# Kernel tuning notes

Hardware: AMD Instinct MI355X
Metric: run time of the kernel (lower is better)

The kernel has to match this reference:

```python
import jax, jax.numpy as jnp
import numpy as np

N = 100000   # nodes
E = 1000000  # edges
F = 64       # in_features == out_features
ALPHA = 0.2  # leaky-relu negative slope


def setup_inputs() -> dict:
    key = jax.random.key(0)
    k = jax.random.split(key, 6)
    h = jax.random.normal(k[0], (N, F), jnp.float32)
    W = jax.random.normal(k[1], (F, F), jnp.float32) * 0.1   # Linear weight [out,in]
    Wb = jnp.zeros((F,), jnp.float32)
    a = jax.random.normal(k[2], (2 * F,), jnp.float32) * 0.1  # attn vector (Linear(2F,1))
    ab = jnp.zeros((), jnp.float32)
    src = jax.random.randint(k[3], (E,), 0, N, dtype=jnp.int32)
    dst = jax.random.randint(k[4], (E,), 0, N, dtype=jnp.int32)
    return {"h": h, "W": W, "Wb": Wb, "a": a, "ab": ab, "src": src, "dst": dst}


def reference(h, W, Wb, a, ab, src, dst):
    # Wh = W(h)  (dropout is identity in eval mode / dropout=0)
    Wh = h @ W.T + Wb                                   # [N, F]
    # e = leakyrelu(a([Wh_src || Wh_dst])) ; split a to avoid concat
    a_src, a_dst = a[:F], a[F:]
    e = jax.nn.leaky_relu(Wh[src] @ a_src + Wh[dst] @ a_dst + ab, ALPHA)  # [E]
    # segment softmax over destination nodes (DGL mailbox softmax)
    m = jax.ops.segment_max(e, dst, num_segments=N)     # [N], -inf for empty
    m = jnp.where(jnp.isfinite(m), m, 0.0)
    ex = jnp.exp(e - m[dst])                            # [E]
    denom = jax.ops.segment_sum(ex, dst, num_segments=N)
    attn = ex / jnp.where(denom[dst] > 0, denom[dst], 1.0)
    # weighted scatter-sum of source features to destinations
    h_prime = jax.ops.segment_sum(attn[:, None] * Wh[src], dst, num_segments=N)  # [N, F]
    return h_prime
```

## Files before the change

kernel.cpp:

```cpp
#include <hip/hip_runtime.h>

#define NF 64
#define ALPHA 0.2f
#define BSH 7
#define BNODES 128
#define CAPG 2048
#define PB 4096
#define HB 800
#define NBIN 1024

typedef unsigned int  uint;
typedef unsigned short ushort;

typedef __attribute__((ext_vector_type(8))) short  short8;
typedef __attribute__((ext_vector_type(4))) float  floatx4;

__device__ __forceinline__ ushort f2bf(float x) {
    uint u = __float_as_uint(x);
    u += 0x7fffu + ((u >> 16) & 1u);
    return (ushort)(u >> 16);
}

__device__ __forceinline__ short8 pack8(float4 lo, float4 hi) {
    short8 r;
    r[0] = (short)f2bf(lo.x); r[1] = (short)f2bf(lo.y);
    r[2] = (short)f2bf(lo.z); r[3] = (short)f2bf(lo.w);
    r[4] = (short)f2bf(hi.x); r[5] = (short)f2bf(hi.y);
    r[6] = (short)f2bf(hi.z); r[7] = (short)f2bf(hi.w);
    return r;
}

__global__ __launch_bounds__(256) void wh_part_kernel(
    const float* __restrict__ h, const float* __restrict__ W,
    const float* __restrict__ Wb, const float* __restrict__ a,
    ushort* __restrict__ whbf, float* __restrict__ s_src, float* __restrict__ s_dst,
    const int* __restrict__ src, const int* __restrict__ dst,
    int* __restrict__ bctr, uint* __restrict__ tmp,
    int N, int E, int edgeB, int NB)
{
    __shared__ uint   stage[PB];
    __shared__ ushort bid[PB];
    __shared__ int    hist[HB];
    __shared__ int    lbase[HB];
    __shared__ int    ctr[HB];
    __shared__ int    gbase[HB];
    __shared__ int    sw[256];

    int t = threadIdx.x;

    if ((int)blockIdx.x < edgeB) {
        int base = (int)blockIdx.x * PB;
        int total = E - base; if (total > PB) total = PB; if (total < 0) total = 0;

        for (int i = t; i < HB; i += 256) hist[i] = 0;
        __syncthreads();

        uint pk[16]; int bb[16];
        #pragma unroll
        for (int g = 0; g < 4; ++g) {
            int ei = base + g * 1024 + t * 4;
            int s4[4], d4[4];
            if (ei + 3 < E) {
                int4 sv = *(const int4*)&src[ei];
                int4 dv = *(const int4*)&dst[ei];
                s4[0]=sv.x; s4[1]=sv.y; s4[2]=sv.z; s4[3]=sv.w;
                d4[0]=dv.x; d4[1]=dv.y; d4[2]=dv.z; d4[3]=dv.w;
            } else {
                #pragma unroll
                for (int j = 0; j < 4; ++j) {
                    int e = ei + j;
                    s4[j] = (e < E) ? src[e] : -1;
                    d4[j] = (e < E) ? dst[e] : -1;
                }
            }
            #pragma unroll
            for (int j = 0; j < 4; ++j) {
                int i16 = g * 4 + j;
                if (d4[j] >= 0) {
                    pk[i16] = ((uint)s4[j] << BSH) | (uint)(d4[j] & (BNODES - 1));
                    bb[i16] = d4[j] >> BSH;
                    atomicAdd(&hist[bb[i16]], 1);
                } else bb[i16] = -1;
            }
        }
        __syncthreads();

        int b0 = t * 4;
        int c0 = 0, c1 = 0, c2 = 0, c3 = 0;
        if (b0 < HB)     c0 = hist[b0];
        if (b0 + 1 < HB) c1 = hist[b0+1];
        if (b0 + 2 < HB) c2 = hist[b0+2];
        if (b0 + 3 < HB) c3 = hist[b0+3];
        int tsum = c0 + c1 + c2 + c3;
        sw[t] = tsum; __syncthreads();
        for (int off = 1; off < 256; off <<= 1) {
            int x = (t >= off) ? sw[t - off] : 0;
            __syncthreads();
            sw[t] += x;
            __syncthreads();
        }
        int ex = sw[t] - tsum;
        if (b0 < HB)     { lbase[b0]   = ex; ex += c0; }
        if (b0 + 1 < HB) { lbase[b0+1] = ex; ex += c1; }
        if (b0 + 2 < HB) { lbase[b0+2] = ex; ex += c2; }
        if (b0 + 3 < HB) { lbase[b0+3] = ex; }
        __syncthreads();

        for (int q = t; q < NB; q += 256) {
            int c = hist[q];
            gbase[q] = c ? atomicAdd(&bctr[q], c) : 0;
            ctr[q] = lbase[q];
        }
        __syncthreads();

        #pragma unroll
        for (int i = 0; i < 16; ++i) {
            if (bb[i] >= 0) {
                int pos = atomicAdd(&ctr[bb[i]], 1);
                stage[pos] = pk[i];
                bid[pos] = (ushort)bb[i];
            }
        }
        __syncthreads();

        for (int i = t; i < total; i += 256) {
            int q = bid[i];
            int off = gbase[q] + (i - lbase[q]);
            if (off < CAPG) tmp[(size_t)q * CAPG + off] = stage[i];
        }
        return;
    }

    int lane = t & 63;
    int wave = t >> 6;
    int r0   = ((int)blockIdx.x - edgeB) * 64 + wave * 16;
    if (r0 >= N) return;
    int m    = lane & 15;
    int quad = lane >> 4;

    short8 bfrag[4][2];
    #pragma unroll
    for (int ct = 0; ct < 4; ++ct) {
        const float* wrow = W + (size_t)(ct * 16 + m) * 64 + quad * 8;
        #pragma unroll
        for (int kh = 0; kh < 2; ++kh) {
            float4 lo = *(const float4*)(wrow + kh * 32);
            float4 hi = *(const float4*)(wrow + kh * 32 + 4);
            bfrag[ct][kh] = pack8(lo, hi);
        }
    }

    int row_a = r0 + m; if (row_a >= N) row_a = N - 1;
    const float* hrow = h + (size_t)row_a * 64 + quad * 8;
    floatx4 zero = {0.f, 0.f, 0.f, 0.f};
    floatx4 acc[4] = {zero, zero, zero, zero};
    #pragma unroll
    for (int kh = 0; kh < 2; ++kh) {
        float4 lo = *(const float4*)(hrow + kh * 32);
        float4 hi = *(const float4*)(hrow + kh * 32 + 4);
        short8 af = pack8(lo, hi);
        #pragma unroll
        for (int ct = 0; ct < 4; ++ct)
            acc[ct] = __builtin_amdgcn_mfma_f32_16x16x32_bf16(af, bfrag[ct][kh], acc[ct], 0, 0, 0);
    }

    float p1[4] = {0.f, 0.f, 0.f, 0.f}, p2[4] = {0.f, 0.f, 0.f, 0.f};
    #pragma unroll
    for (int ct = 0; ct < 4; ++ct) {
        int col = ct * 16 + m;
        float wb  = Wb[col];
        float av1 = a[col];
        float av2 = a[64 + col];
        #pragma unroll
        for (int reg = 0; reg < 4; ++reg) {
            int row = r0 + quad * 4 + reg;
            float v = acc[ct][reg] + wb;
            if (row < N) whbf[(size_t)row * 64 + col] = f2bf(v);
            p1[reg] += v * av1;
            p2[reg] += v * av2;
        }
    }
    #pragma unroll
    for (int off = 8; off >= 1; off >>= 1) {
        #pragma unroll
        for (int reg = 0; reg < 4; ++reg) {
            p1[reg] += __shfl_down(p1[reg], off, 16);
            p2[reg] += __shfl_down(p2[reg], off, 16);
        }
    }
    if (m == 0) {
        #pragma unroll
        for (int reg = 0; reg < 4; ++reg) {
            int row = r0 + quad * 4 + reg;
            if (row < N) { s_src[row] = p1[reg]; s_dst[row] = p2[reg]; }
        }
    }
}

__global__ __launch_bounds__(512) void bucket_aggregate(
    const uint* __restrict__ tmp, const int* __restrict__ bctr,
    const float* __restrict__ s_src, const float* __restrict__ s_dst,
    const float* __restrict__ ab, const ushort* __restrict__ whbf,
    float* __restrict__ out, int N)
{
    __shared__ uint  ssrc[CAPG];
    __shared__ float sexv[CAPG];
    __shared__ int   cnts[NBIN];
    __shared__ int   excl[NBIN + 1];
    __shared__ int   ctr[NBIN];
    __shared__ float sdl[BNODES];

    int t = threadIdx.x;
    int b = blockIdx.x;
    int n0 = b << BSH;
    int cnt = bctr[b]; if (cnt > CAPG) cnt = CAPG;
    float ab0 = ab[0];

    for (int i = t; i < NBIN; i += 512) cnts[i] = 0;
    if (t < BNODES) {
        sdl[t] = (n0 + t < N) ? s_dst[n0 + t] + ab0 : 0.f;
    }
    __syncthreads();

    uint held[4]; int nh = 0;
    #pragma unroll
    for (int j = 0; j < 4; ++j) {
        int idx = t + j * 512;
        if (idx < cnt) {
            uint v = tmp[(size_t)b * CAPG + idx];
            held[nh++] = v;
            int bin = ((v & (BNODES - 1)) << 3) | ((v >> 21) & 7);
            atomicAdd(&cnts[bin], 1);
        }
    }
    __syncthreads();

    if (t < 64) {
        int base16 = t * 16;
        int c[16]; int s = 0;
        #pragma unroll
        for (int k = 0; k < 16; ++k) { c[k] = cnts[base16 + k]; s += c[k]; }
        int incl = s;
        #pragma unroll
        for (int off = 1; off < 64; off <<= 1) {
            int x = __shfl_up(incl, off, 64);
            if (t >= off) incl += x;
        }
        int e = incl - s;
        #pragma unroll
        for (int k = 0; k < 16; ++k) { excl[base16 + k] = e; ctr[base16 + k] = e; e += c[k]; }
        if (t == 63) excl[NBIN] = e;
    }
    __syncthreads();

    #pragma unroll
    for (int j = 0; j < 4; ++j) {
        if (j < nh) {
            uint v = held[j];
            uint s = v >> BSH;
            int node = v & (BNODES - 1);
            float e = s_src[s] + sdl[node];
            e = e > 0.f ? e : ALPHA * e;
            float ex = __expf(e);
            int bin = (node << 3) | ((v >> 21) & 7);
            int pos = atomicAdd(&ctr[bin], 1);
            ssrc[pos] = s; sexv[pos] = ex;
        }
    }
    __syncthreads();

    int g = t >> 3, l8 = t & 7;
    int nlim = N - n0; if (nlim > BNODES) nlim = BNODES;
    int nodeA = g, nodeB = g + 64;
    bool hasA = nodeA < nlim, hasB = nodeB < nlim;

    int a0 = hasA ? excl[nodeA << 3] : 0, a1 = hasA ? excl[(nodeA << 3) + 8] : 0;
    int b0 = hasB ? excl[nodeB << 3] : 0, b1 = hasB ? excl[(nodeB << 3) + 8] : 0;
    int na = a1 - a0, nb = b1 - b0;
    int iters = na > nb ? na : nb;

    float fA[8] = {0.f,0.f,0.f,0.f,0.f,0.f,0.f,0.f};
    float fB[8] = {0.f,0.f,0.f,0.f,0.f,0.f,0.f,0.f};
    float dnA = 0.f, dnB = 0.f;

    if (iters > 0) {
        uint  sA = (na > 0) ? ssrc[a0] : 0u;
        float eA = (na > 0) ? sexv[a0] : 0.f;
        uint4 pA = ((const uint4*)(whbf + (size_t)sA * 64))[l8];
        uint  sB = (nb > 0) ? ssrc[b0] : 0u;
        float eB = (nb > 0) ? sexv[b0] : 0.f;
        uint4 pB = ((const uint4*)(whbf + (size_t)sB * 64))[l8];

        for (int i = 0; i < iters; ++i) {
            int ia = (i + 1 < na) ? a0 + i + 1 : a0;
            int ib = (i + 1 < nb) ? b0 + i + 1 : b0;
            uint  sAn = (i + 1 < na) ? ssrc[ia] : 0u; float eAn = (i + 1 < na) ? sexv[ia] : 0.f;
            uint  sBn = (i + 1 < nb) ? ssrc[ib] : 0u; float eBn = (i + 1 < nb) ? sexv[ib] : 0.f;
            uint4 pAn = ((const uint4*)(whbf + (size_t)sAn * 64))[l8];
            uint4 pBn = ((const uint4*)(whbf + (size_t)sBn * 64))[l8];

            fA[0] += eA * __uint_as_float(pA.x << 16);
            fA[1] += eA * __uint_as_float(pA.x & 0xffff0000u);
            fA[2] += eA * __uint_as_float(pA.y << 16);
            fA[3] += eA * __uint_as_float(pA.y & 0xffff0000u);
            fA[4] += eA * __uint_as_float(pA.z << 16);
            fA[5] += eA * __uint_as_float(pA.z & 0xffff0000u);
            fA[6] += eA * __uint_as_float(pA.w << 16);
            fA[7] += eA * __uint_as_float(pA.w & 0xffff0000u);
            dnA += eA;
            fB[0] += eB * __uint_as_float(pB.x << 16);
            fB[1] += eB * __uint_as_float(pB.x & 0xffff0000u);
            fB[2] += eB * __uint_as_float(pB.y << 16);
            fB[3] += eB * __uint_as_float(pB.y & 0xffff0000u);
            fB[4] += eB * __uint_as_float(pB.z << 16);
            fB[5] += eB * __uint_as_float(pB.z & 0xffff0000u);
            fB[6] += eB * __uint_as_float(pB.w << 16);
            fB[7] += eB * __uint_as_float(pB.w & 0xffff0000u);
            dnB += eB;

            eA = eAn; pA = pAn;
            eB = eBn; pB = pBn;
        }
    }

    if (hasA) {
        float inv = dnA > 0.f ? 1.f / dnA : 1.f;
        float4 o0, o1;
        o0.x = fA[0]*inv; o0.y = fA[1]*inv; o0.z = fA[2]*inv; o0.w = fA[3]*inv;
        o1.x = fA[4]*inv; o1.y = fA[5]*inv; o1.z = fA[6]*inv; o1.w = fA[7]*inv;
        float* orow = out + (size_t)(n0 + nodeA) * 64 + l8 * 8;
        *(float4*)orow       = o0;
        *(float4*)(orow + 4) = o1;
    }
    if (hasB) {
        float inv = dnB > 0.f ? 1.f / dnB : 1.f;
        float4 o0, o1;
        o0.x = fB[0]*inv; o0.y = fB[1]*inv; o0.z = fB[2]*inv; o0.w = fB[3]*inv;
        o1.x = fB[4]*inv; o1.y = fB[5]*inv; o1.z = fB[6]*inv; o1.w = fB[7]*inv;
        float* orow = out + (size_t)(n0 + nodeB) * 64 + l8 * 8;
        *(float4*)orow       = o0;
        *(float4*)(orow + 4) = o1;
    }
}

extern "C" void kernel_launch(void* const* d_in, const int* in_sizes, int n_in,
                              void* d_out, int out_size, void* d_ws, size_t ws_size,
                              hipStream_t stream) {
    const float* h   = (const float*)d_in[0];
    const float* W   = (const float*)d_in[1];
    const float* Wb  = (const float*)d_in[2];
    const float* a   = (const float*)d_in[3];
    const float* ab  = (const float*)d_in[4];
    const int*   src = (const int*)d_in[5];
    const int*   dst = (const int*)d_in[6];

    int N = in_sizes[0] / NF;
    int E = in_sizes[5];
    float* out = (float*)d_out;
    int NB = (N + BNODES - 1) >> BSH;

    ushort* whbf   = (ushort*)d_ws;
    float*  s_src  = (float*)(whbf + (size_t)N * NF);
    float*  s_dst  = s_src + N;
    int*    bctr   = (int*)(s_dst + N);
    uint*   tmp    = (uint*)(bctr + NB);

    hipMemsetAsync(bctr, 0, (size_t)NB * sizeof(int), stream);

    int whB   = (N + 63) / 64;
    int edgeB = (E + PB - 1) / PB;

    wh_part_kernel<<<edgeB + whB, 256, 0, stream>>>(
        h, W, Wb, a, whbf, s_src, s_dst, src, dst, bctr, tmp, N, E, edgeB, NB);

    bucket_aggregate<<<NB, 512, 0, stream>>>(tmp, bctr, s_src, s_dst, ab, whbf, out, N);
}
```

Baseline: 139.9 us.

## Balance aggregation by pairing heavy and light nodes, batch Wh rows per wave

In the aggregation kernel, nodes are ranked by in-degree with a small shared histogram and counting sort. Each 8-lane group then handles the highest- and lowest-ranked nodes one after the other, so its loop runs for the sum of their degrees instead of the maximum of two arbitrary nodes. This is meant to reduce divergence and idle lanes from degree imbalance, at the cost of extra shared-memory passes and barriers. Separately, each Wh wave now processes 64 rows in four batches, so W fragments and the bias and attention vectors are loaded once per 64 rows and fewer blocks are launched.

```diff
diff --git a/kernel.cpp b/kernel.cpp
--- a/kernel.cpp
+++ b/kernel.cpp
@@ -133,7 +133,7 @@
 
     int lane = t & 63;
     int wave = t >> 6;
-    int r0   = ((int)blockIdx.x - edgeB) * 64 + wave * 16;
+    int r0   = ((int)blockIdx.x - edgeB) * 256 + wave * 64;
     if (r0 >= N) return;
     int m    = lane & 15;
     int quad = lane >> 4;
@@ -150,52 +150,76 @@
         }
     }
 
-    int row_a = r0 + m; if (row_a >= N) row_a = N - 1;
-    const float* hrow = h + (size_t)row_a * 64 + quad * 8;
-    floatx4 zero = {0.f, 0.f, 0.f, 0.f};
-    floatx4 acc[4] = {zero, zero, zero, zero};
-    #pragma unroll
-    for (int kh = 0; kh < 2; ++kh) {
-        float4 lo = *(const float4*)(hrow + kh * 32);
-        float4 hi = *(const float4*)(hrow + kh * 32 + 4);
-        short8 af = pack8(lo, hi);
-        #pragma unroll
-        for (int ct = 0; ct < 4; ++ct)
-            acc[ct] = __builtin_amdgcn_mfma_f32_16x16x32_bf16(af, bfrag[ct][kh], acc[ct], 0, 0, 0);
-    }
-
-    float p1[4] = {0.f, 0.f, 0.f, 0.f}, p2[4] = {0.f, 0.f, 0.f, 0.f};
+    float wb4[4], av1_4[4], av2_4[4];
     #pragma unroll
     for (int ct = 0; ct < 4; ++ct) {
         int col = ct * 16 + m;
-        float wb  = Wb[col];
-        float av1 = a[col];
-        float av2 = a[64 + col];
-        #pragma unroll
-        for (int reg = 0; reg < 4; ++reg) {
-            int row = r0 + quad * 4 + reg;
-            float v = acc[ct][reg] + wb;
-            if (row < N) whbf[(size_t)row * 64 + col] = f2bf(v);
-            p1[reg] += v * av1;
-            p2[reg] += v * av2;
-        }
-    }
-    #pragma unroll
-    for (int off = 8; off >= 1; off >>= 1) {
-        #pragma unroll
-        for (int reg = 0; reg < 4; ++reg) {
-            p1[reg] += __shfl_down(p1[reg], off, 16);
-            p2[reg] += __shfl_down(p2[reg], off, 16);
-        }
-    }
-    if (m == 0) {
-        #pragma unroll
-        for (int reg = 0; reg < 4; ++reg) {
-            int row = r0 + quad * 4 + reg;
-            if (row < N) { s_src[row] = p1[reg]; s_dst[row] = p2[reg]; }
+        wb4[ct]   = Wb[col];
+        av1_4[ct] = a[col];
+        av2_4[ct] = a[64 + col];
+    }
+
+    for (int batch = 0; batch < 4; ++batch) {
+        int rb = r0 + batch * 16;
+        if (rb >= N) break;
+
+        int row_a = rb + m; if (row_a >= N) row_a = N - 1;
+        const float* hrow = h + (size_t)row_a * 64 + quad * 8;
+        floatx4 zero = {0.f, 0.f, 0.f, 0.f};
+        floatx4 acc[4] = {zero, zero, zero, zero};
+        #pragma unroll
+        for (int kh = 0; kh < 2; ++kh) {
+            float4 lo = *(const float4*)(hrow + kh * 32);
+            float4 hi = *(const float4*)(hrow + kh * 32 + 4);
+            short8 af = pack8(lo, hi);
+            #pragma unroll
+            for (int ct = 0; ct < 4; ++ct)
+                acc[ct] = __builtin_amdgcn_mfma_f32_16x16x32_bf16(af, bfrag[ct][kh], acc[ct], 0, 0, 0);
+        }
+
+        float p1[4] = {0.f, 0.f, 0.f, 0.f}, p2[4] = {0.f, 0.f, 0.f, 0.f};
+        #pragma unroll
+        for (int ct = 0; ct < 4; ++ct) {
+            int col = ct * 16 + m;
+            #pragma unroll
+            for (int reg = 0; reg < 4; ++reg) {
+                int row = rb + quad * 4 + reg;
+                float v = acc[ct][reg] + wb4[ct];
+                if (row < N) whbf[(size_t)row * 64 + col] = f2bf(v);
+                p1[reg] += v * av1_4[ct];
+                p2[reg] += v * av2_4[ct];
+            }
+        }
+        #pragma unroll
+        for (int off = 8; off >= 1; off >>= 1) {
+            #pragma unroll
+            for (int reg = 0; reg < 4; ++reg) {
+                p1[reg] += __shfl_down(p1[reg], off, 16);
+                p2[reg] += __shfl_down(p2[reg], off, 16);
+            }
+        }
+        if (m == 0) {
+            #pragma unroll
+            for (int reg = 0; reg < 4; ++reg) {
+                int row = rb + quad * 4 + reg;
+                if (row < N) { s_src[row] = p1[reg]; s_dst[row] = p2[reg]; }
+            }
         }
     }
 }
+
+#define STOREROW(node_, f_, dn_)                                          \
+    if ((node_) < nlim) {                                                 \
+        float inv_ = (dn_) > 0.f ? 1.f / (dn_) : 1.f;                     \
+        float* orow_ = out + (size_t)(n0 + (node_)) * 64 + l8 * 8;        \
+        float4 o0_, o1_;                                                  \
+        o0_.x = f_[0]*inv_; o0_.y = f_[1]*inv_;                           \
+        o0_.z = f_[2]*inv_; o0_.w = f_[3]*inv_;                           \
+        o1_.x = f_[4]*inv_; o1_.y = f_[5]*inv_;                           \
+        o1_.z = f_[6]*inv_; o1_.w = f_[7]*inv_;                           \
+        *(float4*)orow_       = o0_;                                      \
+        *(float4*)(orow_ + 4) = o1_;                                      \
+    }
 
 __global__ __launch_bounds__(512) void bucket_aggregate(
     const uint* __restrict__ tmp, const int* __restrict__ bctr,
@@ -203,12 +227,14 @@
     const float* __restrict__ ab, const ushort* __restrict__ whbf,
     float* __restrict__ out, int N)
 {
-    __shared__ uint  ssrc[CAPG];
-    __shared__ float sexv[CAPG];
-    __shared__ int   cnts[NBIN];
-    __shared__ int   excl[NBIN + 1];
-    __shared__ int   ctr[NBIN];
-    __shared__ float sdl[BNODES];
+    __shared__ uint   ssrc[CAPG];
+    __shared__ float  sexv[CAPG];
+    __shared__ int    cnts[NBIN];
+    __shared__ int    excl[NBIN + 1];
+    __shared__ int    ctr[NBIN];
+    __shared__ float  sdl[BNODES];
+    __shared__ int    chist[64];
+    __shared__ ushort rk[BNODES];
 
     int t = threadIdx.x;
     int b = blockIdx.x;
@@ -220,6 +246,7 @@
     if (t < BNODES) {
         sdl[t] = (n0 + t < N) ? s_dst[n0 + t] + ab0 : 0.f;
     }
+    if (t >= BNODES && t < BNODES + 64) chist[t - BNODES] = 0;
     __syncthreads();
 
     uint held[4]; int nh = 0;
@@ -252,6 +279,12 @@
         if (t == 63) excl[NBIN] = e;
     }
     __syncthreads();
+
+    int myCnt = 0;
+    if (t < BNODES) {
+        myCnt = excl[(t << 3) + 8] - excl[t << 3];
+        atomicAdd(&chist[myCnt > 63 ? 63 : myCnt], 1);
+    }
 
     #pragma unroll
     for (int j = 0; j < 4; ++j) {
@@ -269,78 +302,78 @@
     }
     __syncthreads();
 
+    if (t < 64) {
+        int c = chist[t];
+        int incl = c;
+        #pragma unroll
+        for (int off = 1; off < 64; off <<= 1) {
+            int x = __shfl_up(incl, off, 64);
+            if (t >= off) incl += x;
+        }
+        chist[t] = incl - c;
+    }
+    __syncthreads();
+    if (t < BNODES) {
+        int r = atomicAdd(&chist[myCnt > 63 ? 63 : myCnt], 1);
+        rk[r] = (ushort)t;
+    }
+    __syncthreads();
+
     int g = t >> 3, l8 = t & 7;
     int nlim = N - n0; if (nlim > BNODES) nlim = BNODES;
-    int nodeA = g, nodeB = g + 64;
-    bool hasA = nodeA < nlim, hasB = nodeB < nlim;
-
-    int a0 = hasA ? excl[nodeA << 3] : 0, a1 = hasA ? excl[(nodeA << 3) + 8] : 0;
-    int b0 = hasB ? excl[nodeB << 3] : 0, b1 = hasB ? excl[(nodeB << 3) + 8] : 0;
-    int na = a1 - a0, nb = b1 - b0;
-    int iters = na > nb ? na : nb;
-
-    float fA[8] = {0.f,0.f,0.f,0.f,0.f,0.f,0.f,0.f};
-    float fB[8] = {0.f,0.f,0.f,0.f,0.f,0.f,0.f,0.f};
-    float dnA = 0.f, dnB = 0.f;
-
-    if (iters > 0) {
-        uint  sA = (na > 0) ? ssrc[a0] : 0u;
-        float eA = (na > 0) ? sexv[a0] : 0.f;
-        uint4 pA = ((const uint4*)(whbf + (size_t)sA * 64))[l8];
-        uint  sB = (nb > 0) ? ssrc[b0] : 0u;
-        float eB = (nb > 0) ? sexv[b0] : 0.f;
-        uint4 pB = ((const uint4*)(whbf + (size_t)sB * 64))[l8];
-
-        for (int i = 0; i < iters; ++i) {
-            int ia = (i + 1 < na) ? a0 + i + 1 : a0;
-            int ib = (i + 1 < nb) ? b0 + i + 1 : b0;
-            uint  sAn = (i + 1 < na) ? ssrc[ia] : 0u; float eAn = (i + 1 < na) ? sexv[ia] : 0.f;
-            uint  sBn = (i + 1 < nb) ? ssrc[ib] : 0u; float eBn = (i + 1 < nb) ? sexv[ib] : 0.f;
-            uint4 pAn = ((const uint4*)(whbf + (size_t)sAn * 64))[l8];
-            uint4 pBn = ((const uint4*)(whbf + (size_t)sBn * 64))[l8];
-
-            fA[0] += eA * __uint_as_float(pA.x << 16);
-            fA[1] += eA * __uint_as_float(pA.x & 0xffff0000u);
-            fA[2] += eA * __uint_as_float(pA.y << 16);
-            fA[3] += eA * __uint_as_float(pA.y & 0xffff0000u);
-            fA[4] += eA * __uint_as_float(pA.z << 16);
-            fA[5] += eA * __uint_as_float(pA.z & 0xffff0000u);
-            fA[6] += eA * __uint_as_float(pA.w << 16);
-            fA[7] += eA * __uint_as_float(pA.w & 0xffff0000u);
-            dnA += eA;
-            fB[0] += eB * __uint_as_float(pB.x << 16);
-            fB[1] += eB * __uint_as_float(pB.x & 0xffff0000u);
-            fB[2] += eB * __uint_as_float(pB.y << 16);
-            fB[3] += eB * __uint_as_float(pB.y & 0xffff0000u);
-            fB[4] += eB * __uint_as_float(pB.z << 16);
-            fB[5] += eB * __uint_as_float(pB.z & 0xffff0000u);
-            fB[6] += eB * __uint_as_float(pB.w << 16);
-            fB[7] += eB * __uint_as_float(pB.w & 0xffff0000u);
-            dnB += eB;
-
-            eA = eAn; pA = pAn;
-            eB = eBn; pB = pBn;
-        }
-    }
-
-    if (hasA) {
-        float inv = dnA > 0.f ? 1.f / dnA : 1.f;
-        float4 o0, o1;
-        o0.x = fA[0]*inv; o0.y = fA[1]*inv; o0.z = fA[2]*inv; o0.w = fA[3]*inv;
-        o1.x = fA[4]*inv; o1.y = fA[5]*inv; o1.z = fA[6]*inv; o1.w = fA[7]*inv;
-        float* orow = out + (size_t)(n0 + nodeA) * 64 + l8 * 8;
-        *(float4*)orow       = o0;
-        *(float4*)(orow + 4) = o1;
-    }
-    if (hasB) {
-        float inv = dnB > 0.f ? 1.f / dnB : 1.f;
-        float4 o0, o1;
-        o0.x = fB[0]*inv; o0.y = fB[1]*inv; o0.z = fB[2]*inv; o0.w = fB[3]*inv;
-        o1.x = fB[4]*inv; o1.y = fB[5]*inv; o1.z = fB[6]*inv; o1.w = fB[7]*inv;
-        float* orow = out + (size_t)(n0 + nodeB) * 64 + l8 * 8;
-        *(float4*)orow       = o0;
-        *(float4*)(orow + 4) = o1;
-    }
+    int nodeP = rk[127 - g];
+    int nodeQ = rk[g];
+
+    int p0 = excl[nodeP << 3], nP = excl[(nodeP << 3) + 8] - p0;
+    int q0 = excl[nodeQ << 3], nQ = excl[(nodeQ << 3) + 8] - q0;
+    int total = nP + nQ;
+
+    float f[8] = {0.f,0.f,0.f,0.f,0.f,0.f,0.f,0.f};
+    float dn = 0.f;
+    bool pDone = false;
+
+    if (total > 0) {
+        int i0 = (0 < nP) ? p0 : q0;
+        float eC = sexv[i0];
+        uint  sC = ssrc[i0];
+        uint4 pC = ((const uint4*)(whbf + (size_t)sC * 64))[l8];
+
+        for (int i = 0; i < total; ++i) {
+            int nx = i + 1;
+            int ix = (nx < total) ? ((nx < nP) ? p0 + nx : q0 + nx - nP) : 0;
+            uint  sN = ssrc[ix];
+            float eN = sexv[ix];
+            uint4 pN = ((const uint4*)(whbf + (size_t)sN * 64))[l8];
+
+            if (!pDone && i == nP) {
+                STOREROW(nodeP, f, dn);
+                #pragma unroll
+                for (int k = 0; k < 8; ++k) f[k] = 0.f;
+                dn = 0.f;
+                pDone = true;
+            }
+
+            f[0] += eC * __uint_as_float(pC.x << 16);
+            f[1] += eC * __uint_as_float(pC.x & 0xffff0000u);
+            f[2] += eC * __uint_as_float(pC.y << 16);
+            f[3] += eC * __uint_as_float(pC.y & 0xffff0000u);
+            f[4] += eC * __uint_as_float(pC.z << 16);
+            f[5] += eC * __uint_as_float(pC.z & 0xffff0000u);
+            f[6] += eC * __uint_as_float(pC.w << 16);
+            f[7] += eC * __uint_as_float(pC.w & 0xffff0000u);
+            dn += eC;
+
+            eC = eN; pC = pN;
+        }
+    }
+
+    if (!pDone) {
+        STOREROW(nodeP, f, dn);
+        #pragma unroll
+        for (int k = 0; k < 8; ++k) f[k] = 0.f;
+        dn = 0.f;
+    }
+    STOREROW(nodeQ, f, dn);
 }
 
 extern "C" void kernel_launch(void* const* d_in, const int* in_sizes, int n_in,
@@ -367,7 +400,7 @@
 
     hipMemsetAsync(bctr, 0, (size_t)NB * sizeof(int), stream);
 
-    int whB   = (N + 63) / 64;
+    int whB   = (N + 255) / 256;
     int edgeB = (E + PB - 1) / PB;
 
     wh_part_kernel<<<edgeB + whB, 256, 0, stream>>>(
```

New measurement: 131.1 us (median of 2 runs). 1.07x faster.
